# Kernel tuning notes

Measured on AMD Instinct MI355X. Metric: run time of the kernel, lower is better.

The kernel has to match this reference:

```python
import jax, jax.numpy as jnp
import numpy as np

NUM_EXPERTS = 8
HIDDEN = 2048
EXPERT_DIM = 2048  # intermediate_size per shard (tp_size=1)
TOTAL_TOKENS = 32768  # divisible by NUM_EXPERTS


def setup_inputs() -> dict:
    key = jax.random.key(0)
    k1, k2, k3 = jax.random.split(key, 3)
    hidden_states = jax.random.normal(k1, (TOTAL_TOKENS, HIDDEN), dtype=jnp.float32)
    # (E, H, 2*D): gate and up projections concatenated on last dim
    gate_up_proj = jax.random.normal(k2, (NUM_EXPERTS, HIDDEN, 2 * EXPERT_DIM), dtype=jnp.float32) * 0.02
    # (E, D, H)
    down_proj = jax.random.normal(k3, (NUM_EXPERTS, EXPERT_DIM, HIDDEN), dtype=jnp.float32) * 0.02
    return {"hidden_states": hidden_states, "gate_up_proj": gate_up_proj, "down_proj": down_proj}


def reference(hidden_states, gate_up_proj, down_proj):
    E, H = gate_up_proj.shape[0], gate_up_proj.shape[1]
    # tokens are pre-sorted per expert: (E, T, H)
    x = hidden_states.reshape(E, -1, H)
    # grouped GEMM: (E,T,H) @ (E,H,2D) -> (E,T,2D)
    gate_up = jnp.einsum('eth,ehd->etd', x, gate_up_proj)
    gate, up = jnp.split(gate_up, 2, axis=-1)
    # SwiGLU epilogue then down projection: (E,T,D) @ (E,D,H) -> (E,T,H)
    act = up * jax.nn.silu(gate)
    out = jnp.einsum('etd,edh->eth', act, down_proj)
    # tp_size=1 -> all_reduce is identity
    return out.reshape(-1, H)
```

## Files before the change

kernel.cpp:

```cpp
#include <hip/hip_runtime.h>


#define E_EXPERTS 8
#define TPE 4096
#define KD 2048

typedef __bf16 bf16_t;
typedef __bf16 bf16x4 __attribute__((ext_vector_type(4)));
typedef __bf16 bf16x8 __attribute__((ext_vector_type(8)));
typedef float f32x4 __attribute__((ext_vector_type(4)));

#define GLOAD16(src, dst)                                               \
  __builtin_amdgcn_global_load_lds(                                     \
      (const __attribute__((address_space(1))) void*)(src),             \
      (__attribute__((address_space(3))) void*)(dst), 16, 0, 0)

__global__ void cvt_f32_bf16_kernel(const float* __restrict__ in,
                                    bf16_t* __restrict__ out, long n4) {
  long i = (long)blockIdx.x * blockDim.x + threadIdx.x;
  const long stride = (long)gridDim.x * blockDim.x;
  const float4* in4 = (const float4*)in;
  bf16x4* out4 = (bf16x4*)out;
  for (; i < n4; i += stride) {
    float4 v = in4[i];
    bf16x4 o = {(bf16_t)v.x, (bf16_t)v.y, (bf16_t)v.z, (bf16_t)v.w};
    out4[i] = o;
  }
}

__global__ void transpose_cvt_kernel(const float* __restrict__ W,
                                     bf16_t* __restrict__ WT, int K, int N) {
  __shared__ float tile[64][65];
  const int e = blockIdx.z;
  const float* Wp = W + (size_t)e * K * N;
  bf16_t* Tp = WT + (size_t)e * N * K;
  const int n0 = blockIdx.x * 64, k0 = blockIdx.y * 64;
  const int rr = threadIdx.x >> 4;
  const int cc = (threadIdx.x & 15) * 4;
#pragma unroll
  for (int p = 0; p < 4; ++p) {
    const int k = rr + p * 16;
    float4 v = *(const float4*)(Wp + (size_t)(k0 + k) * N + n0 + cc);
    tile[k][cc + 0] = v.x;
    tile[k][cc + 1] = v.y;
    tile[k][cc + 2] = v.z;
    tile[k][cc + 3] = v.w;
  }
  __syncthreads();
#pragma unroll
  for (int p = 0; p < 4; ++p) {
    const int n = rr + p * 16;
    bf16x4 o;
#pragma unroll
    for (int j = 0; j < 4; ++j) o[j] = (bf16_t)tile[cc + j][n];
    *(bf16x4*)(Tp + (size_t)(n0 + n) * K + k0 + cc) = o;
  }
}

template <bool FUSED, int NTN>
__global__ __launch_bounds__(512, 4) void moe_gemm128_kernel(
    const bf16_t* __restrict__ A, const bf16_t* __restrict__ Bm,
    void* __restrict__ Cout) {
  constexpr int NT = KD / 64;

  __shared__ alignas(16) bf16_t As[2][128][64];
  __shared__ alignas(16) bf16_t Bs[2][128][64];

  const int NWG = gridDim.x;
  int wg = blockIdx.x;
  wg = (wg & 7) * (NWG >> 3) + (wg >> 3);
  const int per = 32 * NTN;
  const int e = wg / per;
  const int rem = wg % per;
  const int mt = rem / NTN, ntile = rem % NTN;
  const int t0 = mt * 128, n0 = ntile * 128;

  const int tid = threadIdx.x;
  const int wid = tid >> 6, lane = tid & 63;
  const int wr = wid >> 2, wc = wid & 3;

  const bf16_t* Ae = A + (size_t)e * TPE * KD + (size_t)t0 * KD;
  const bf16_t* Be = Bm + (size_t)e * (size_t)(FUSED ? 4096 : 2048) * KD;

  const int slr = lane >> 3;
  const int sel = ((lane & 7) ^ slr) * 8;

  auto stageA = [&](int kt, int h) {
    const int ktw = kt & (NT - 1);
    const int k0 = ktw * 64;
    const int buf = kt & 1;
    const int r0 = h * 64 + wid * 8;
    GLOAD16(Ae + (size_t)(r0 + slr) * KD + k0 + sel, &As[buf][r0][0]);
  };
  auto stageB = [&](int kt, int h) {
    const int ktw = kt & (NT - 1);
    const int k0 = ktw * 64;
    const int buf = kt & 1;
    const int r0 = h * 64 + wid * 8;
    const int R = n0 + r0 + slr;
    int srow;
    if constexpr (FUSED)
      srow = ((R >> 5) << 4) + (R & 15) + ((R >> 4) & 1) * 2048;
    else
      srow = R;
    GLOAD16(Be + (size_t)srow * KD + k0 + sel, &Bs[buf][r0][0]);
  };

  const int la = lane & 15, kg4 = lane >> 4;

  f32x4 acc[4][2] = {};
  bf16x8 afP[2][2], afQ[2][2];
  bf16x8 bX[2], bY[2];

  auto readAm = [&](int buf, int mp, bf16x8 (&dst)[2][2]) {
#pragma unroll
    for (int mm = 0; mm < 2; ++mm) {
      const int row = wr * 64 + mp * 32 + mm * 16 + la;
#pragma unroll
      for (int kk = 0; kk < 2; ++kk) {
        const int ch = ((kk * 4 + kg4) ^ (la & 7)) * 8;
        dst[mm][kk] = *(const bf16x8*)&As[buf][row][ch];
      }
    }
  };
  auto readBn = [&](int buf, int nf, bf16x8 (&dst)[2]) {
    const int row = wc * 32 + nf * 16 + la;
#pragma unroll
    for (int kk = 0; kk < 2; ++kk) {
      const int ch = ((kk * 4 + kg4) ^ (la & 7)) * 8;
      dst[kk] = *(const bf16x8*)&Bs[buf][row][ch];
    }
  };

#define W6 asm volatile("s_waitcnt lgkmcnt(6)" ::: "memory")
#define W4 asm volatile("s_waitcnt lgkmcnt(4)" ::: "memory")
#define W0 asm volatile("s_waitcnt lgkmcnt(0)" ::: "memory")
#define VMC2 asm volatile("s_waitcnt vmcnt(2)" ::: "memory")
#define BAR __builtin_amdgcn_s_barrier()
#define SCHED0 __builtin_amdgcn_sched_barrier(0)
#define PRIO1 __builtin_amdgcn_s_setprio(1)
#define PRIO0 __builtin_amdgcn_s_setprio(0)

#define MMA_H(AF, NF, BF)                                                   \
  do {                                                                      \
    _Pragma("unroll") for (int kk = 0; kk < 2; ++kk) {                      \
      _Pragma("unroll") for (int mm = 0; mm < 2; ++mm) {                    \
        accp[mm][NF] = __builtin_amdgcn_mfma_f32_16x16x32_bf16(             \
            AF[mm][kk], BF[kk], accp[mm][NF], 0, 0, 0);                     \
      }                                                                     \
    }                                                                       \
  } while (0)

#define TILE(kt, buf)                                                       \
  do {                                                                      \
    \
    readAm(buf, 0, afP);                                                    \
    readBn(buf, 0, bX);                                                     \
    readBn(buf, 1, bY);                                                     \
    readAm(buf, 1, afQ);                                                    \
    stageA((kt) + 1, 0);                                                    \
    W6; SCHED0;                                                             \
    { auto& accp = accL;                                                    \
      PRIO1; MMA_H(afP, 0, bX); PRIO0;                                      \
                                                                    \
      stageA((kt) + 1, 1);                                                  \
      W4; SCHED0;                                                           \
      PRIO1; MMA_H(afP, 1, bY); PRIO0;                                      \
      BAR; }                                                                \
                                                                    \
    stageB((kt) + 2, 0);                                                    \
    W0; SCHED0;                                                             \
    { auto& accp = accH;                                                    \
      PRIO1; MMA_H(afQ, 1, bY); PRIO0;                                      \
                                                                    \
      stageB((kt) + 2, 1);                                                  \
      PRIO1; MMA_H(afQ, 0, bX); PRIO0; }                                    \
    VMC2;                                                                   \
    BAR;                                                                    \
  } while (0)

  auto accL = (f32x4(*)[2]) & acc[0];
  auto accH = (f32x4(*)[2]) & acc[2];

  stageA(0, 0); stageA(0, 1);
  stageB(0, 0); stageB(0, 1);
  stageB(1, 0); stageB(1, 1);
  VMC2;
  BAR;

  for (int kt = 0; kt < NT; kt += 2) {
    TILE(kt, 0);
    TILE(kt + 1, 1);
  }

  const int lg = lane >> 4;
  const int rbase = t0 + wr * 64;
  if constexpr (FUSED) {
    bf16_t* Cp = (bf16_t*)Cout + (size_t)e * TPE * KD;
    const int jb = (n0 + wc * 32) >> 1;
#pragma unroll
    for (int m = 0; m < 4; ++m)
#pragma unroll
      for (int r = 0; r < 4; ++r) {
        const int row = rbase + m * 16 + lg * 4 + r;
        const int col = jb + la;
        const float g = acc[m][0][r], u = acc[m][1][r];
        const float s = 1.0f / (1.0f + __expf(-g));
        Cp[(size_t)row * KD + col] = (bf16_t)(u * g * s);
      }
  } else {
    float* Cp = (float*)Cout + (size_t)e * TPE * KD;
#pragma unroll
    for (int m = 0; m < 4; ++m)
#pragma unroll
      for (int n = 0; n < 2; ++n)
#pragma unroll
        for (int r = 0; r < 4; ++r) {
          const int row = rbase + m * 16 + lg * 4 + r;
          const int col = n0 + wc * 32 + n * 16 + la;
          Cp[(size_t)row * KD + col] = acc[m][n][r];
        }
  }
#undef W6
#undef W4
#undef W0
#undef VMC2
#undef BAR
#undef SCHED0
#undef PRIO1
#undef PRIO0
#undef MMA_H
#undef TILE
}

extern "C" void kernel_launch(void* const* d_in, const int* in_sizes, int n_in,
                              void* d_out, int out_size, void* d_ws,
                              size_t ws_size, hipStream_t stream) {
  const float* hs = (const float*)d_in[0];
  const float* w1 = (const float*)d_in[1];
  const float* w2 = (const float*)d_in[2];

  char* ws = (char*)d_ws;
  bf16_t* xb = (bf16_t*)(ws);
  bf16_t* w1t = (bf16_t*)(ws + (size_t)134217728);
  bf16_t* w2t = (bf16_t*)(ws + (size_t)268435456);
  bf16_t* act = (bf16_t*)(ws + (size_t)335544320);

  const long n4 = (long)E_EXPERTS * TPE * KD / 4;
  cvt_f32_bf16_kernel<<<2048, 256, 0, stream>>>(hs, xb, n4);
  transpose_cvt_kernel<<<dim3(64, 32, 8), 256, 0, stream>>>(w1, w1t, 2048, 4096);
  transpose_cvt_kernel<<<dim3(32, 32, 8), 256, 0, stream>>>(w2, w2t, 2048, 2048);
  moe_gemm128_kernel<true, 32><<<8192, 512, 0, stream>>>(xb, w1t, (void*)act);
  moe_gemm128_kernel<false, 16><<<4096, 512, 0, stream>>>(act, w2t, d_out);
}
```

Measured before the change: 1.289 ms.

## Switch MoE GEMMs to 256x256 tiles with 32x32 MFMA and 4-stage pipeline

Replaces the 128x128-tile, 512-thread grouped GEMM with a 256x256-tile, 1024-thread (16-wave) kernel that uses 32x32x16 bf16 MFMA, a K-step of 32 and a 4-deep LDS ring buffer with three tiles in flight. The larger tile is meant to raise arithmetic intensity and cut global/LDS traffic per flop, and the deeper pipeline is meant to hide load latency better. The gate/up row interleave and the SwiGLU epilogue are remapped to the new 32-wide fragment layout. In exchange it issues twice as many barriers per unit of K, uses fewer, larger workgroups (which may hurt occupancy and tail balance), and keeps 64 accumulator floats per lane.

New measurement: 1.411 ms. 1.09x slower.

```diff
diff --git a/kernel.cpp b/kernel.cpp
--- a/kernel.cpp
+++ b/kernel.cpp
@@ -8,7 +8,7 @@
 typedef __bf16 bf16_t;
 typedef __bf16 bf16x4 __attribute__((ext_vector_type(4)));
 typedef __bf16 bf16x8 __attribute__((ext_vector_type(8)));
-typedef float f32x4 __attribute__((ext_vector_type(4)));
+typedef float f32x16 __attribute__((ext_vector_type(16)));
 
 #define GLOAD16(src, dst)                                               \
   __builtin_amdgcn_global_load_lds(                                     \
@@ -58,179 +58,156 @@
 }
 
 template <bool FUSED, int NTN>
-__global__ __launch_bounds__(512, 4) void moe_gemm128_kernel(
+__global__ __launch_bounds__(1024, 4) void moe_gemm32_kernel(
     const bf16_t* __restrict__ A, const bf16_t* __restrict__ Bm,
     void* __restrict__ Cout) {
-  constexpr int NT = KD / 64;
-
-  __shared__ alignas(16) bf16_t As[2][128][64];
-  __shared__ alignas(16) bf16_t Bs[2][128][64];
+  constexpr int NT = KD / 32;
+
+  __shared__ alignas(16) bf16_t As[4][256][32];
+  __shared__ alignas(16) bf16_t Bs[4][256][32];
 
   const int NWG = gridDim.x;
   int wg = blockIdx.x;
   wg = (wg & 7) * (NWG >> 3) + (wg >> 3);
-  const int per = 32 * NTN;
-  const int e = wg / per;
-  const int rem = wg % per;
+  const int e = wg / (16 * NTN);
+  const int rem = wg % (16 * NTN);
   const int mt = rem / NTN, ntile = rem % NTN;
-  const int t0 = mt * 128, n0 = ntile * 128;
+  const int t0 = mt * 256, n0 = ntile * 256;
 
   const int tid = threadIdx.x;
   const int wid = tid >> 6, lane = tid & 63;
-  const int wr = wid >> 2, wc = wid & 3;
+  const int wm = wid >> 1, wn = wid & 1;
 
   const bf16_t* Ae = A + (size_t)e * TPE * KD + (size_t)t0 * KD;
   const bf16_t* Be = Bm + (size_t)e * (size_t)(FUSED ? 4096 : 2048) * KD;
 
-  const int slr = lane >> 3;
-  const int sel = ((lane & 7) ^ slr) * 8;
-
-  auto stageA = [&](int kt, int h) {
-    const int ktw = kt & (NT - 1);
-    const int k0 = ktw * 64;
-    const int buf = kt & 1;
-    const int r0 = h * 64 + wid * 8;
-    GLOAD16(Ae + (size_t)(r0 + slr) * KD + k0 + sel, &As[buf][r0][0]);
-  };
-  auto stageB = [&](int kt, int h) {
-    const int ktw = kt & (NT - 1);
-    const int k0 = ktw * 64;
-    const int buf = kt & 1;
-    const int r0 = h * 64 + wid * 8;
+  const int slr = lane >> 2;
+  const int sel = ((lane & 3) ^ (slr & 3)) * 8;
+
+  auto stageA = [&](int kt, int bD) {
+    const int k0 = (kt & (NT - 1)) * 32;
+    const int r0 = wid * 16;
+    GLOAD16(Ae + (size_t)(r0 + slr) * KD + k0 + sel, &As[bD][r0][0]);
+  };
+  auto stageB = [&](int kt, int bD) {
+    const int k0 = (kt & (NT - 1)) * 32;
+    const int r0 = wid * 16;
     const int R = n0 + r0 + slr;
     int srow;
     if constexpr (FUSED)
-      srow = ((R >> 5) << 4) + (R & 15) + ((R >> 4) & 1) * 2048;
+      srow = ((R >> 6) << 5) + (R & 31) + ((R >> 5) & 1) * 2048;
     else
       srow = R;
-    GLOAD16(Be + (size_t)srow * KD + k0 + sel, &Bs[buf][r0][0]);
-  };
-
-  const int la = lane & 15, kg4 = lane >> 4;
-
-  f32x4 acc[4][2] = {};
-  bf16x8 afP[2][2], afQ[2][2];
-  bf16x8 bX[2], bY[2];
-
-  auto readAm = [&](int buf, int mp, bf16x8 (&dst)[2][2]) {
-#pragma unroll
-    for (int mm = 0; mm < 2; ++mm) {
-      const int row = wr * 64 + mp * 32 + mm * 16 + la;
-#pragma unroll
-      for (int kk = 0; kk < 2; ++kk) {
-        const int ch = ((kk * 4 + kg4) ^ (la & 7)) * 8;
-        dst[mm][kk] = *(const bf16x8*)&As[buf][row][ch];
-      }
-    }
-  };
-  auto readBn = [&](int buf, int nf, bf16x8 (&dst)[2]) {
-    const int row = wc * 32 + nf * 16 + la;
-#pragma unroll
-    for (int kk = 0; kk < 2; ++kk) {
-      const int ch = ((kk * 4 + kg4) ^ (la & 7)) * 8;
-      dst[kk] = *(const bf16x8*)&Bs[buf][row][ch];
+    GLOAD16(Be + (size_t)srow * KD + k0 + sel, &Bs[bD][r0][0]);
+  };
+
+  const int l31 = lane & 31, l3 = lane & 3, hk = lane >> 5;
+
+  f32x16 acc[4] = {};
+  bf16x8 aS[2];
+  bf16x8 b0[2], b1[2], b2[2], b3[2];
+
+  auto readA = [&](int bR) {
+    const int row = wm * 32 + l31;
+#pragma unroll
+    for (int s = 0; s < 2; ++s) {
+      const int ch = ((2 * s + hk) ^ l3) * 8;
+      aS[s] = *(const bf16x8*)&As[bR][row][ch];
+    }
+  };
+  auto readB = [&](int bR, int qn, bf16x8 (&dst)[2]) {
+    const int row = wn * 128 + qn * 32 + l31;
+#pragma unroll
+    for (int s = 0; s < 2; ++s) {
+      const int ch = ((2 * s + hk) ^ l3) * 8;
+      dst[s] = *(const bf16x8*)&Bs[bR][row][ch];
     }
   };
 
 #define W6 asm volatile("s_waitcnt lgkmcnt(6)" ::: "memory")
 #define W4 asm volatile("s_waitcnt lgkmcnt(4)" ::: "memory")
+#define W2 asm volatile("s_waitcnt lgkmcnt(2)" ::: "memory")
 #define W0 asm volatile("s_waitcnt lgkmcnt(0)" ::: "memory")
-#define VMC2 asm volatile("s_waitcnt vmcnt(2)" ::: "memory")
+#define VMC4 asm volatile("s_waitcnt vmcnt(4)" ::: "memory")
 #define BAR __builtin_amdgcn_s_barrier()
 #define SCHED0 __builtin_amdgcn_sched_barrier(0)
 #define PRIO1 __builtin_amdgcn_s_setprio(1)
 #define PRIO0 __builtin_amdgcn_s_setprio(0)
-
-#define MMA_H(AF, NF, BF)                                                   \
-  do {                                                                      \
-    _Pragma("unroll") for (int kk = 0; kk < 2; ++kk) {                      \
-      _Pragma("unroll") for (int mm = 0; mm < 2; ++mm) {                    \
-        accp[mm][NF] = __builtin_amdgcn_mfma_f32_16x16x32_bf16(             \
-            AF[mm][kk], BF[kk], accp[mm][NF], 0, 0, 0);                     \
-      }                                                                     \
-    }                                                                       \
+#define MMA(Q, B)                                                     \
+  do {                                                                \
+    acc[Q] = __builtin_amdgcn_mfma_f32_32x32x16_bf16(aS[0], B[0],     \
+                                                     acc[Q], 0, 0, 0); \
+    acc[Q] = __builtin_amdgcn_mfma_f32_32x32x16_bf16(aS[1], B[1],     \
+                                                     acc[Q], 0, 0, 0); \
   } while (0)
 
-#define TILE(kt, buf)                                                       \
-  do {                                                                      \
-    \
-    readAm(buf, 0, afP);                                                    \
-    readBn(buf, 0, bX);                                                     \
-    readBn(buf, 1, bY);                                                     \
-    readAm(buf, 1, afQ);                                                    \
-    stageA((kt) + 1, 0);                                                    \
-    W6; SCHED0;                                                             \
-    { auto& accp = accL;                                                    \
-      PRIO1; MMA_H(afP, 0, bX); PRIO0;                                      \
-                                                                    \
-      stageA((kt) + 1, 1);                                                  \
-      W4; SCHED0;                                                           \
-      PRIO1; MMA_H(afP, 1, bY); PRIO0;                                      \
-      BAR; }                                                                \
-                                                                    \
-    stageB((kt) + 2, 0);                                                    \
-    W0; SCHED0;                                                             \
-    { auto& accp = accH;                                                    \
-      PRIO1; MMA_H(afQ, 1, bY); PRIO0;                                      \
-                                                                    \
-      stageB((kt) + 2, 1);                                                  \
-      PRIO1; MMA_H(afQ, 0, bX); PRIO0; }                                    \
-    VMC2;                                                                   \
-    BAR;                                                                    \
-  } while (0)
-
-  auto accL = (f32x4(*)[2]) & acc[0];
-  auto accH = (f32x4(*)[2]) & acc[2];
-
-  stageA(0, 0); stageA(0, 1);
-  stageB(0, 0); stageB(0, 1);
-  stageB(1, 0); stageB(1, 1);
-  VMC2;
-  BAR;
-
-  for (int kt = 0; kt < NT; kt += 2) {
-    TILE(kt, 0);
-    TILE(kt + 1, 1);
-  }
-
-  const int lg = lane >> 4;
-  const int rbase = t0 + wr * 64;
+  stageA(0, 0); stageB(0, 0);
+  stageA(1, 1); stageB(1, 1);
+  stageA(2, 2); stageB(2, 2);
+  VMC4;
+  BAR; SCHED0;
+
+  int bR = 0;
+  for (int t = 0; t < NT; ++t) {
+    const int bD = (bR + 3) & 3;
+    readA(bR);
+    readB(bR, 0, b0);
+    readB(bR, 1, b1);
+    readB(bR, 2, b2);
+    readB(bR, 3, b3);
+    stageA(t + 3, bD);
+    stageB(t + 3, bD);
+    W6; SCHED0;
+    PRIO1; MMA(0, b0); PRIO0;
+    W4; SCHED0;
+    PRIO1; MMA(1, b1); PRIO0;
+    BAR;
+    W2; SCHED0;
+    PRIO1; MMA(2, b2); PRIO0;
+    W0; SCHED0;
+    PRIO1; MMA(3, b3); PRIO0;
+    VMC4;
+    BAR; SCHED0;
+    bR = (bR + 1) & 3;
+  }
+
+  const int rbase = t0 + wm * 32;
   if constexpr (FUSED) {
     bf16_t* Cp = (bf16_t*)Cout + (size_t)e * TPE * KD;
-    const int jb = (n0 + wc * 32) >> 1;
-#pragma unroll
-    for (int m = 0; m < 4; ++m)
-#pragma unroll
-      for (int r = 0; r < 4; ++r) {
-        const int row = rbase + m * 16 + lg * 4 + r;
-        const int col = jb + la;
-        const float g = acc[m][0][r], u = acc[m][1][r];
+    const int d0 = ((n0 + wn * 128) >> 1) + l31;
+#pragma unroll
+    for (int p = 0; p < 2; ++p) {
+#pragma unroll
+      for (int reg = 0; reg < 16; ++reg) {
+        const int row = rbase + (reg & 3) + 8 * (reg >> 2) + 4 * hk;
+        const int col = d0 + p * 32;
+        const float g = acc[2 * p][reg], u = acc[2 * p + 1][reg];
         const float s = 1.0f / (1.0f + __expf(-g));
         Cp[(size_t)row * KD + col] = (bf16_t)(u * g * s);
       }
+    }
   } else {
     float* Cp = (float*)Cout + (size_t)e * TPE * KD;
 #pragma unroll
-    for (int m = 0; m < 4; ++m)
-#pragma unroll
-      for (int n = 0; n < 2; ++n)
-#pragma unroll
-        for (int r = 0; r < 4; ++r) {
-          const int row = rbase + m * 16 + lg * 4 + r;
-          const int col = n0 + wc * 32 + n * 16 + la;
-          Cp[(size_t)row * KD + col] = acc[m][n][r];
-        }
+    for (int q = 0; q < 4; ++q) {
+#pragma unroll
+      for (int reg = 0; reg < 16; ++reg) {
+        const int row = rbase + (reg & 3) + 8 * (reg >> 2) + 4 * hk;
+        const int col = n0 + wn * 128 + q * 32 + l31;
+        Cp[(size_t)row * KD + col] = acc[q][reg];
+      }
+    }
   }
 #undef W6
 #undef W4
+#undef W2
 #undef W0
-#undef VMC2
+#undef VMC4
 #undef BAR
 #undef SCHED0
 #undef PRIO1
 #undef PRIO0
-#undef MMA_H
-#undef TILE
+#undef MMA
 }
 
 extern "C" void kernel_launch(void* const* d_in, const int* in_sizes, int n_in,
@@ -250,6 +227,6 @@
   cvt_f32_bf16_kernel<<<2048, 256, 0, stream>>>(hs, xb, n4);
   transpose_cvt_kernel<<<dim3(64, 32, 8), 256, 0, stream>>>(w1, w1t, 2048, 4096);
   transpose_cvt_kernel<<<dim3(32, 32, 8), 256, 0, stream>>>(w2, w2t, 2048, 2048);
-  moe_gemm128_kernel<true, 32><<<8192, 512, 0, stream>>>(xb, w1t, (void*)act);
-  moe_gemm128_kernel<false, 16><<<4096, 512, 0, stream>>>(act, w2t, d_out);
-}
+  moe_gemm32_kernel<true, 16><<<2048, 1024, 0, stream>>>(xb, w1t, (void*)act);
+  moe_gemm32_kernel<false, 8><<<1024, 1024, 0, stream>>>(act, w2t, d_out);
+}
```
